# Performance work log

Measured on AMD Instinct MI355X. Metric: run time of the kernel, lower is better.

## Reference

```python
import jax, jax.numpy as jnp
import numpy as np

B, T, N = 32, 2048, 2048
D, L, TE, H = 512, 256, 1024, 8

def _ln(x, g, b, eps=1e-5):
    m = x.mean(-1, keepdims=True)
    v = ((x - m) ** 2).mean(-1, keepdims=True)
    return (x - m) / jnp.sqrt(v + eps) * g + b

def setup_inputs() -> dict:
    key = jax.random.key(0)
    ks = jax.random.split(key, 12)
    s = 0.02
    return {
        "x": jax.random.normal(ks[0], (B, T, D), jnp.float32),
        "xf": jax.random.normal(ks[1], (B, N, L), jnp.float32),
        "emb": jax.random.normal(ks[2], (B, TE), jnp.float32),
        "norm_g": jnp.ones((D,), jnp.float32),
        "norm_b": jnp.zeros((D,), jnp.float32),
        "tnorm_g": jnp.ones((L,), jnp.float32),
        "tnorm_b": jnp.zeros((L,), jnp.float32),
        "Wq": jax.random.normal(ks[3], (D, D), jnp.float32) * s,
        "bq": jnp.zeros((D,), jnp.float32),
        "Wk": jax.random.normal(ks[4], (L, D), jnp.float32) * s,
        "bk": jnp.zeros((D,), jnp.float32),
        "Wv": jax.random.normal(ks[5], (L, D), jnp.float32) * s,
        "bv": jnp.zeros((D,), jnp.float32),
        "We": jax.random.normal(ks[6], (TE, 2 * D), jnp.float32) * s,
        "be": jnp.zeros((2 * D,), jnp.float32),
        "snorm_g": jnp.ones((D,), jnp.float32),
        "snorm_b": jnp.zeros((D,), jnp.float32),
        "Wo": jax.random.normal(ks[7], (D, D), jnp.float32) * s,
        "bo": jnp.zeros((D,), jnp.float32),
    }

def reference(x, xf, emb, norm_g, norm_b, tnorm_g, tnorm_b, Wq, bq, Wk, bk, Wv, bv,
              We, be, snorm_g, snorm_b, Wo, bo):
    b, t, d = x.shape
    n = xf.shape[1]
    hd = d // H
    # projections with pre-LayerNorms
    q = (_ln(x, norm_g, norm_b) @ Wq + bq).reshape(b, t, H, hd)
    xfn = _ln(xf, tnorm_g, tnorm_b)
    k = (xfn @ Wk + bk).reshape(b, n, H, hd)
    v = (xfn @ Wv + bv).reshape(b, n, H, hd)
    # dual softmax of linear attention: query over head-dim, key over sequence
    q = jax.nn.softmax(q, axis=-1)
    k = jax.nn.softmax(k, axis=1)
    # O(N*d^2) linear attention
    attn = jnp.einsum('bnhd,bnhl->bhdl', k, v)          # [B,H,hd,hd]
    y = jnp.einsum('bthd,bhdl->bthl', q, attn).reshape(b, t, d)
    # StylizationBlock (dropout is identity in eval)
    emb_out = jax.nn.silu(emb) @ We + be                # [B, 2D]
    scale, shift = emb_out[:, None, :d], emb_out[:, None, d:]
    h = _ln(y, snorm_g, snorm_b) * (1.0 + scale) + shift
    h = jax.nn.silu(h) @ Wo + bo
    return x + h
```

## Files before the change

### kernel.cpp

```cpp
#include <hip/hip_runtime.h>
#include <math.h>

#define B_ 32
#define T_ 2048
#define N_ 2048
#define D_ 512
#define L_ 256
#define TE_ 1024
#define H_ 8
#define MROWS 65536
#define KCH 16
#define NC_ 8

typedef __attribute__((ext_vector_type(8))) short short8;
typedef __attribute__((ext_vector_type(4))) float f32x4;

__device__ __forceinline__ unsigned short f2bf(float f) {
  unsigned u = __float_as_uint(f);
  unsigned r = (u + 0x7FFF + ((u >> 16) & 1)) >> 16;
  return (unsigned short)r;
}
__device__ __forceinline__ float bf2f(unsigned short u) {
  return __uint_as_float(((unsigned)u) << 16);
}
__device__ __forceinline__ void gload_lds16(const void* g, void* l) {
  __builtin_amdgcn_global_load_lds(
      (const __attribute__((address_space(1))) void*)g,
      (__attribute__((address_space(3))) void*)l, 16, 0, 0);
}

__device__ __forceinline__ float blockReduceSum(float v, float* ws) {
#pragma unroll
  for (int m = 32; m >= 1; m >>= 1) v += __shfl_xor(v, m, 64);
  int wid = threadIdx.x >> 6;
  int lane = threadIdx.x & 63;
  __syncthreads();
  if (lane == 0) ws[wid] = v;
  __syncthreads();
  return ws[0] + ws[1] + ws[2] + ws[3];
}

template <int COLS>
__global__ void __launch_bounds__(256) ln_rows(const float* __restrict__ in,
                                               const float* __restrict__ g,
                                               const float* __restrict__ bb,
                                               unsigned short* __restrict__ out) {
  constexpr int E = COLS / 256;
  __shared__ float ws[4];
  size_t row = blockIdx.x;
  const float* rp = in + row * COLS;
  float v[E];
  float s = 0.f;
#pragma unroll
  for (int e = 0; e < E; ++e) {
    v[e] = rp[threadIdx.x + e * 256];
    s += v[e];
  }
  s = blockReduceSum(s, ws);
  float mean = s * (1.0f / COLS);
  float q = 0.f;
#pragma unroll
  for (int e = 0; e < E; ++e) {
    float d = v[e] - mean;
    q += d * d;
  }
  q = blockReduceSum(q, ws);
  float rstd = rsqrtf(q * (1.0f / COLS) + 1e-5f);
  unsigned short* op = out + row * COLS;
#pragma unroll
  for (int e = 0; e < E; ++e) {
    int c = threadIdx.x + e * 256;
    op[c] = f2bf((v[e] - mean) * rstd * g[c] + bb[c]);
  }
}

__global__ void __launch_bounds__(256) transcast(const float* __restrict__ W,
                                                 unsigned short* __restrict__ Wt,
                                                 int K, int Ncols) {
  __shared__ float t[32][33];
  int k0 = blockIdx.x * 32, n0 = blockIdx.y * 32;
  int tx = threadIdx.x & 31, ty = threadIdx.x >> 5;
#pragma unroll
  for (int i = 0; i < 32; i += 8)
    t[ty + i][tx] = W[(size_t)(k0 + ty + i) * Ncols + n0 + tx];
  __syncthreads();
#pragma unroll
  for (int i = 0; i < 32; i += 8)
    Wt[(size_t)(n0 + ty + i) * K + k0 + tx] = f2bf(t[tx][ty + i]);
}

template <int KT, bool ADD, bool OUTBF>
__global__ void __launch_bounds__(256) gemm_mfma(const unsigned short* __restrict__ A,
                                                 const unsigned short* __restrict__ Wt,
                                                 const float* __restrict__ bias,
                                                 const float* __restrict__ add,
                                                 void* __restrict__ Cv) {
  __shared__ __align__(16) unsigned short sA[128 * 32];
  __shared__ __align__(16) unsigned short sB[128 * 32];
  int tid = threadIdx.x;
  int w = tid >> 6, lane = tid & 63;
  int quad = lane >> 4, r16 = lane & 15;
  int wr = w >> 1, wc = w & 1;
  size_t m0 = (size_t)blockIdx.y * 128;
  int n0 = blockIdx.x * 128;
  int srow = lane >> 2;
  int scol = (lane & 3) * 8;
  f32x4 acc[4][4] = {};

  for (int k0 = 0; k0 < KT; k0 += 32) {
    __syncthreads();
#pragma unroll
    for (int i = 0; i < 2; ++i) {
      int seg = w * 2 + i;
      gload_lds16(&A[(m0 + seg * 16 + srow) * KT + k0 + scol], &sA[seg * 512]);
    }
#pragma unroll
    for (int i = 0; i < 2; ++i) {
      int seg = w * 2 + i;
      gload_lds16(&Wt[(size_t)(n0 + seg * 16 + srow) * KT + k0 + scol], &sB[seg * 512]);
    }
    __syncthreads();
    short8 af[4], bfr[4];
#pragma unroll
    for (int mi = 0; mi < 4; ++mi)
      af[mi] = *(const short8*)&sA[(wr * 64 + mi * 16 + r16) * 32 + quad * 8];
#pragma unroll
    for (int ni = 0; ni < 4; ++ni)
      bfr[ni] = *(const short8*)&sB[(wc * 64 + ni * 16 + r16) * 32 + quad * 8];
#pragma unroll
    for (int mi = 0; mi < 4; ++mi)
#pragma unroll
      for (int ni = 0; ni < 4; ++ni)
        acc[mi][ni] = __builtin_amdgcn_mfma_f32_16x16x32_bf16(af[mi], bfr[ni], acc[mi][ni], 0, 0, 0);
  }

  float* Cf = (float*)Cv;
  unsigned short* Cb = (unsigned short*)Cv;
#pragma unroll
  for (int mi = 0; mi < 4; ++mi)
#pragma unroll
    for (int r = 0; r < 4; ++r) {
      size_t grow = m0 + wr * 64 + mi * 16 + quad * 4 + r;
#pragma unroll
      for (int ni = 0; ni < 4; ++ni) {
        int gcol = n0 + wc * 64 + ni * 16 + r16;
        float val = acc[mi][ni][r] + bias[gcol];
        if constexpr (ADD) val += add[grow * 512 + gcol];
        if constexpr (OUTBF)
          Cb[grow * 512 + gcol] = f2bf(val);
        else
          Cf[grow * 512 + gcol] = val;
      }
    }
}

__global__ void __launch_bounds__(256) kstats_part(const float* __restrict__ k,
                                                   float* __restrict__ pmax,
                                                   float* __restrict__ psum) {
  int b = blockIdx.x, cg = blockIdx.y, ch = blockIdx.z;
  int tid = threadIdx.x;
  int lane = tid & 63, slice = tid >> 6;
  int c = cg * 64 + lane;
  constexpr int ROWS = N_ / KCH;
  constexpr int PT = ROWS / 4;
  const float* kp = k + ((size_t)b * N_ + (size_t)ch * ROWS) * D_ + c;
  float v[PT];
#pragma unroll
  for (int i = 0; i < PT; ++i) v[i] = kp[(size_t)(slice + i * 4) * D_];
  float m = v[0];
#pragma unroll
  for (int i = 1; i < PT; ++i) m = fmaxf(m, v[i]);
  float s = 0.f;
#pragma unroll
  for (int i = 0; i < PT; ++i) s += expf(v[i] - m);
  __shared__ float mred[256], sred[256];
  mred[tid] = m;
  sred[tid] = s;
  __syncthreads();
  if (tid < 64) {
    float m0 = mred[tid], m1 = mred[tid + 64], m2 = mred[tid + 128], m3 = mred[tid + 192];
    float mm = fmaxf(fmaxf(m0, m1), fmaxf(m2, m3));
    float ss = sred[tid] * expf(m0 - mm) + sred[tid + 64] * expf(m1 - mm) +
               sred[tid + 128] * expf(m2 - mm) + sred[tid + 192] * expf(m3 - mm);
    pmax[((size_t)b * KCH + ch) * D_ + cg * 64 + tid] = mm;
    psum[((size_t)b * KCH + ch) * D_ + cg * 64 + tid] = ss;
  }
}

__global__ void __launch_bounds__(256) kstats_comb(const float* __restrict__ pmax,
                                                   const float* __restrict__ psum,
                                                   float* __restrict__ kmax,
                                                   float* __restrict__ ksum) {
  int b = blockIdx.x;
  int c = blockIdx.y * 256 + threadIdx.x;
  float pm[KCH];
#pragma unroll
  for (int ch = 0; ch < KCH; ++ch) pm[ch] = pmax[((size_t)b * KCH + ch) * D_ + c];
  float m = pm[0];
#pragma unroll
  for (int ch = 1; ch < KCH; ++ch) m = fmaxf(m, pm[ch]);
  float s = 0.f;
#pragma unroll
  for (int ch = 0; ch < KCH; ++ch)
    s += psum[((size_t)b * KCH + ch) * D_ + c] * expf(pm[ch] - m);
  kmax[b * D_ + c] = m;
  ksum[b * D_ + c] = s;
}

__global__ void __launch_bounds__(256) attn_part_kernel(const float* __restrict__ k,
                                                        const float* __restrict__ v,
                                                        const float* __restrict__ kmax,
                                                        const float* __restrict__ ksum,
                                                        float* __restrict__ part) {
  int b = blockIdx.x, h = blockIdx.y, nc = blockIdx.z;
  int tid = threadIdx.x;
  __shared__ float ks_[32][68];
  __shared__ float vs_[32][68];
  __shared__ float mx[64], is_[64];
  if (tid < 64) {
    mx[tid] = kmax[b * D_ + h * 64 + tid];
    is_[tid] = 1.f / ksum[b * D_ + h * 64 + tid];
  }
  const float* kp = k + ((size_t)b * N_ + nc * 256) * D_ + h * 64;
  const float* vp = v + ((size_t)b * N_ + nc * 256) * D_ + h * 64;
  float acc[4][4] = {};
  int tx = tid & 15, ty = tid >> 4;
  int lr = tid >> 4;
  int c4 = (tid & 15) * 4;
  for (int n0 = 0; n0 < 256; n0 += 32) {
    __syncthreads();
#pragma unroll
    for (int rr = 0; rr < 32; rr += 16) {
      float4 kv = *(const float4*)&kp[(size_t)(n0 + lr + rr) * D_ + c4];
      float4 vv = *(const float4*)&vp[(size_t)(n0 + lr + rr) * D_ + c4];
      ks_[lr + rr][c4 + 0] = expf(kv.x - mx[c4 + 0]) * is_[c4 + 0];
      ks_[lr + rr][c4 + 1] = expf(kv.y - mx[c4 + 1]) * is_[c4 + 1];
      ks_[lr + rr][c4 + 2] = expf(kv.z - mx[c4 + 2]) * is_[c4 + 2];
      ks_[lr + rr][c4 + 3] = expf(kv.w - mx[c4 + 3]) * is_[c4 + 3];
      vs_[lr + rr][c4 + 0] = vv.x;
      vs_[lr + rr][c4 + 1] = vv.y;
      vs_[lr + rr][c4 + 2] = vv.z;
      vs_[lr + rr][c4 + 3] = vv.w;
    }
    __syncthreads();
#pragma unroll
    for (int nn = 0; nn < 32; ++nn) {
      float av[4], bv2[4];
#pragma unroll
      for (int i = 0; i < 4; ++i) av[i] = ks_[nn][ty * 4 + i];
#pragma unroll
      for (int j = 0; j < 4; ++j) bv2[j] = vs_[nn][tx * 4 + j];
#pragma unroll
      for (int i = 0; i < 4; ++i)
#pragma unroll
        for (int j = 0; j < 4; ++j) acc[i][j] += av[i] * bv2[j];
    }
  }
  float* ap = part + ((size_t)(b * H_ + h) * NC_ + nc) * 4096;
#pragma unroll
  for (int i = 0; i < 4; ++i) {
    float4 st = make_float4(acc[i][0], acc[i][1], acc[i][2], acc[i][3]);
    *(float4*)&ap[(ty * 4 + i) * 64 + tx * 4] = st;
  }
}

__global__ void __launch_bounds__(256) attn_reduce(const float* __restrict__ part,
                                                   float* __restrict__ attn) {
  size_t o = ((size_t)blockIdx.x * 256 + threadIdx.x) * 4;
  size_t bh = o >> 12;
  size_t e = o & 4095;
  float4 s = make_float4(0.f, 0.f, 0.f, 0.f);
#pragma unroll
  for (int nc = 0; nc < NC_; ++nc) {
    float4 p = *(const float4*)&part[(bh * NC_ + nc) * 4096 + e];
    s.x += p.x;
    s.y += p.y;
    s.z += p.z;
    s.w += p.w;
  }
  *(float4*)&attn[o] = s;
}

__global__ void __launch_bounds__(256) embmod(const float* __restrict__ emb,
                                              const float* __restrict__ We,
                                              const float* __restrict__ be,
                                              float* __restrict__ eo) {
  int b = blockIdx.x, tid = threadIdx.x;
  __shared__ float se[TE_];
  for (int i = tid; i < TE_; i += 256) {
    float e = emb[b * TE_ + i];
    se[i] = e / (1.f + expf(-e));
  }
  __syncthreads();
  int j0 = tid * 4;
  float a0 = 0, a1 = 0, a2 = 0, a3 = 0;
  for (int i = 0; i < TE_; ++i) {
    float s = se[i];
    float4 wv = *(const float4*)&We[(size_t)i * 1024 + j0];
    a0 += s * wv.x;
    a1 += s * wv.y;
    a2 += s * wv.z;
    a3 += s * wv.w;
  }
  eo[b * 1024 + j0 + 0] = a0 + be[j0 + 0];
  eo[b * 1024 + j0 + 1] = a1 + be[j0 + 1];
  eo[b * 1024 + j0 + 2] = a2 + be[j0 + 2];
  eo[b * 1024 + j0 + 3] = a3 + be[j0 + 3];
}

__global__ void __launch_bounds__(256) yein(const unsigned short* __restrict__ q,
                                            const float* __restrict__ attn,
                                            float* __restrict__ y) {
  int t0 = blockIdx.x * 32, h = blockIdx.y, b = blockIdx.z;
  int tid = threadIdx.x;
  __shared__ float at[64][68];
  __shared__ float qs[32][68];
  const float* ap = attn + (size_t)(b * H_ + h) * 4096;
  for (int i = tid; i < 4096; i += 256) at[i >> 6][i & 63] = ap[i];
  const unsigned short* qp = q + ((size_t)b * T_ + t0) * D_ + h * 64;
  for (int i = tid; i < 2048; i += 256)
    qs[i >> 6][i & 63] = bf2f(qp[(size_t)(i >> 6) * D_ + (i & 63)]);
  __syncthreads();
  int r = tid >> 3, c0 = (tid & 7) * 8;
  float lv[8];
#pragma unroll
  for (int j = 0; j < 8; ++j) lv[j] = qs[r][c0 + j];
  float m = lv[0];
#pragma unroll
  for (int j = 1; j < 8; ++j) m = fmaxf(m, lv[j]);
#pragma unroll
  for (int s = 4; s >= 1; s >>= 1) m = fmaxf(m, __shfl_xor(m, s, 64));
  float ssum = 0.f;
#pragma unroll
  for (int j = 0; j < 8; ++j) {
    lv[j] = expf(lv[j] - m);
    ssum += lv[j];
  }
#pragma unroll
  for (int s = 4; s >= 1; s >>= 1) ssum += __shfl_xor(ssum, s, 64);
  float inv = 1.f / ssum;
#pragma unroll
  for (int j = 0; j < 8; ++j) qs[r][c0 + j] = lv[j];
  __syncthreads();
  float acc[8] = {};
#pragma unroll
  for (int d = 0; d < 64; ++d) {
    float qv = qs[r][d];
#pragma unroll
    for (int j = 0; j < 8; ++j) acc[j] += qv * at[d][c0 + j];
  }
  float* yp = y + ((size_t)b * T_ + t0 + r) * D_ + h * 64 + c0;
#pragma unroll
  for (int j = 0; j < 8; ++j) yp[j] = acc[j] * inv;
}

__global__ void __launch_bounds__(256) modln(const float* __restrict__ y,
                                             const float* __restrict__ sg,
                                             const float* __restrict__ sb,
                                             const float* __restrict__ eo,
                                             unsigned short* __restrict__ hs) {
  __shared__ float ws[4];
  size_t row = blockIdx.x;
  int b = (int)(row >> 11);
  const float* rp = y + row * D_;
  float v[2];
  float s = 0.f;
#pragma unroll
  for (int e = 0; e < 2; ++e) {
    v[e] = rp[threadIdx.x + e * 256];
    s += v[e];
  }
  s = blockReduceSum(s, ws);
  float mean = s * (1.0f / D_);
  float q = 0.f;
#pragma unroll
  for (int e = 0; e < 2; ++e) {
    float d = v[e] - mean;
    q += d * d;
  }
  q = blockReduceSum(q, ws);
  float rstd = rsqrtf(q * (1.0f / D_) + 1e-5f);
#pragma unroll
  for (int e = 0; e < 2; ++e) {
    int c = threadIdx.x + e * 256;
    float xm = (v[e] - mean) * rstd * sg[c] + sb[c];
    float sc = eo[b * 1024 + c];
    float sh = eo[b * 1024 + D_ + c];
    float hm = xm * (1.f + sc) + sh;
    hs[row * D_ + c] = f2bf(hm / (1.f + expf(-hm)));
  }
}

extern "C" void kernel_launch(void* const* d_in, const int* in_sizes, int n_in,
                              void* d_out, int out_size, void* d_ws, size_t ws_size,
                              hipStream_t stream) {
  const float* x = (const float*)d_in[0];
  const float* xf = (const float*)d_in[1];
  const float* emb = (const float*)d_in[2];
  const float* norm_g = (const float*)d_in[3];
  const float* norm_b = (const float*)d_in[4];
  const float* tnorm_g = (const float*)d_in[5];
  const float* tnorm_b = (const float*)d_in[6];
  const float* Wq = (const float*)d_in[7];
  const float* bq = (const float*)d_in[8];
  const float* Wk = (const float*)d_in[9];
  const float* bk = (const float*)d_in[10];
  const float* Wv = (const float*)d_in[11];
  const float* bv = (const float*)d_in[12];
  const float* We = (const float*)d_in[13];
  const float* be = (const float*)d_in[14];
  const float* sg = (const float*)d_in[15];
  const float* sb = (const float*)d_in[16];
  const float* Wo = (const float*)d_in[17];
  const float* bo = (const float*)d_in[18];
  float* out = (float*)d_out;

  float* w = (float*)d_ws;
  unsigned short* qbf = (unsigned short*)w;
  float* kbuf = w + 16777216;
  float* vbuf = w + 16777216 + 33554432;
  unsigned short* xnbf = (unsigned short*)(w + 83886080);
  unsigned short* xfnbf = (unsigned short*)(w + 100663296);
  float* attn = w + 109051904;
  float* kmaxp = attn + 1048576;
  float* ksump = kmaxp + 16384;
  float* embout = ksump + 16384;
  unsigned short* wqt = (unsigned short*)(embout + 32768);
  unsigned short* wkt = wqt + 262144;
  unsigned short* wvt = wkt + 131072;
  unsigned short* wot = wvt + 131072;
  float* pmaxp = w + 83886080;
  float* psump = pmaxp + (size_t)B_ * KCH * D_;
  float* attnpart = w + 100663296;

  transcast<<<dim3(16, 16), 256, 0, stream>>>(Wq, wqt, 512, 512);
  transcast<<<dim3(8, 16), 256, 0, stream>>>(Wk, wkt, 256, 512);
  transcast<<<dim3(8, 16), 256, 0, stream>>>(Wv, wvt, 256, 512);
  transcast<<<dim3(16, 16), 256, 0, stream>>>(Wo, wot, 512, 512);
  ln_rows<512><<<MROWS, 256, 0, stream>>>(x, norm_g, norm_b, xnbf);
  gemm_mfma<512, false, true><<<dim3(4, 512), 256, 0, stream>>>(xnbf, wqt, bq, nullptr, qbf);
  ln_rows<256><<<MROWS, 256, 0, stream>>>(xf, tnorm_g, tnorm_b, xfnbf);
  gemm_mfma<256, false, false><<<dim3(4, 512), 256, 0, stream>>>(xfnbf, wkt, bk, nullptr, kbuf);
  gemm_mfma<256, false, false><<<dim3(4, 512), 256, 0, stream>>>(xfnbf, wvt, bv, nullptr, vbuf);
  kstats_part<<<dim3(32, 8, KCH), 256, 0, stream>>>(kbuf, pmaxp, psump);
  kstats_comb<<<dim3(32, 2), 256, 0, stream>>>(pmaxp, psump, kmaxp, ksump);
  attn_part_kernel<<<dim3(32, 8, NC_), 256, 0, stream>>>(kbuf, vbuf, kmaxp, ksump, attnpart);
  attn_reduce<<<1024, 256, 0, stream>>>(attnpart, attn);
  embmod<<<32, 256, 0, stream>>>(emb, We, be, embout);
  yein<<<dim3(64, 8, 32), 256, 0, stream>>>(qbf, attn, kbuf);
  modln<<<MROWS, 256, 0, stream>>>(kbuf, sg, sb, embout, xnbf);
  gemm_mfma<512, true, false><<<dim3(4, 512), 256, 0, stream>>>(xnbf, wot, bo, x, out);
}
```

Baseline: 946.0 us.

## Fuse query softmax into Q GEMM epilogue and run y-einsum on MFMA

The per-head query softmax now runs in the Q projection GEMM epilogue, using cross-lane shuffles over the 64 columns each wave holds for a head, and writes normalized bf16 q. attn_reduce writes the attention matrix transposed in bf16, so a new MFMA kernel (yein_mfma) can compute q·attn with bf16 matrix instructions instead of the scalar FP32 loop. This removes the softmax pass and the scalar FMA work from the yein stage. In exchange, the attention matrix and the post-softmax q are rounded to bf16, which costs some accuracy.

Result: no change. 941.1 us (-0.5%).

```diff
diff --git a/kernel.cpp b/kernel.cpp
--- a/kernel.cpp
+++ b/kernel.cpp
@@ -89,7 +89,7 @@
     Wt[(size_t)(n0 + ty + i) * K + k0 + tx] = f2bf(t[tx][ty + i]);
 }
 
-template <int KT, bool ADD, bool OUTBF>
+template <int KT, bool ADD, bool OUTBF, bool QSM>
 __global__ void __launch_bounds__(256) gemm_mfma(const unsigned short* __restrict__ A,
                                                  const unsigned short* __restrict__ Wt,
                                                  const float* __restrict__ bias,
@@ -141,15 +141,41 @@
 #pragma unroll
     for (int r = 0; r < 4; ++r) {
       size_t grow = m0 + wr * 64 + mi * 16 + quad * 4 + r;
-#pragma unroll
-      for (int ni = 0; ni < 4; ++ni) {
-        int gcol = n0 + wc * 64 + ni * 16 + r16;
-        float val = acc[mi][ni][r] + bias[gcol];
-        if constexpr (ADD) val += add[grow * 512 + gcol];
-        if constexpr (OUTBF)
-          Cb[grow * 512 + gcol] = f2bf(val);
-        else
-          Cf[grow * 512 + gcol] = val;
+      if constexpr (QSM) {
+        float v4[4];
+        float mx = -1e30f;
+#pragma unroll
+        for (int ni = 0; ni < 4; ++ni) {
+          v4[ni] = acc[mi][ni][r] + bias[n0 + wc * 64 + ni * 16 + r16];
+          mx = fmaxf(mx, v4[ni]);
+        }
+#pragma unroll
+        for (int s = 8; s >= 1; s >>= 1) mx = fmaxf(mx, __shfl_xor(mx, s, 64));
+        float ssum = 0.f;
+#pragma unroll
+        for (int ni = 0; ni < 4; ++ni) {
+          v4[ni] = expf(v4[ni] - mx);
+          ssum += v4[ni];
+        }
+#pragma unroll
+        for (int s = 8; s >= 1; s >>= 1) ssum += __shfl_xor(ssum, s, 64);
+        float inv = 1.f / ssum;
+#pragma unroll
+        for (int ni = 0; ni < 4; ++ni) {
+          int gcol = n0 + wc * 64 + ni * 16 + r16;
+          Cb[grow * 512 + gcol] = f2bf(v4[ni] * inv);
+        }
+      } else {
+#pragma unroll
+        for (int ni = 0; ni < 4; ++ni) {
+          int gcol = n0 + wc * 64 + ni * 16 + r16;
+          float val = acc[mi][ni][r] + bias[gcol];
+          if constexpr (ADD) val += add[grow * 512 + gcol];
+          if constexpr (OUTBF)
+            Cb[grow * 512 + gcol] = f2bf(val);
+          else
+            Cf[grow * 512 + gcol] = val;
+        }
       }
     }
 }
@@ -265,7 +291,7 @@
 }
 
 __global__ void __launch_bounds__(256) attn_reduce(const float* __restrict__ part,
-                                                   float* __restrict__ attn) {
+                                                   unsigned short* __restrict__ attnT) {
   size_t o = ((size_t)blockIdx.x * 256 + threadIdx.x) * 4;
   size_t bh = o >> 12;
   size_t e = o & 4095;
@@ -278,7 +304,13 @@
     s.z += p.z;
     s.w += p.w;
   }
-  *(float4*)&attn[o] = s;
+  int d = (int)(e >> 6);
+  int l = (int)(e & 63);
+  unsigned short* ab = attnT + bh * 4096;
+  ab[(l + 0) * 64 + d] = f2bf(s.x);
+  ab[(l + 1) * 64 + d] = f2bf(s.y);
+  ab[(l + 2) * 64 + d] = f2bf(s.z);
+  ab[(l + 3) * 64 + d] = f2bf(s.w);
 }
 
 __global__ void __launch_bounds__(256) embmod(const float* __restrict__ emb,
@@ -308,50 +340,54 @@
   eo[b * 1024 + j0 + 3] = a3 + be[j0 + 3];
 }
 
-__global__ void __launch_bounds__(256) yein(const unsigned short* __restrict__ q,
-                                            const float* __restrict__ attn,
-                                            float* __restrict__ y) {
-  int t0 = blockIdx.x * 32, h = blockIdx.y, b = blockIdx.z;
+__global__ void __launch_bounds__(256) yein_mfma(const unsigned short* __restrict__ qsm,
+                                                 const unsigned short* __restrict__ attnT,
+                                                 float* __restrict__ y) {
+  int b = blockIdx.z, h = blockIdx.y;
+  size_t t0 = (size_t)blockIdx.x * 256;
   int tid = threadIdx.x;
-  __shared__ float at[64][68];
-  __shared__ float qs[32][68];
-  const float* ap = attn + (size_t)(b * H_ + h) * 4096;
-  for (int i = tid; i < 4096; i += 256) at[i >> 6][i & 63] = ap[i];
-  const unsigned short* qp = q + ((size_t)b * T_ + t0) * D_ + h * 64;
-  for (int i = tid; i < 2048; i += 256)
-    qs[i >> 6][i & 63] = bf2f(qp[(size_t)(i >> 6) * D_ + (i & 63)]);
-  __syncthreads();
-  int r = tid >> 3, c0 = (tid & 7) * 8;
-  float lv[8];
-#pragma unroll
-  for (int j = 0; j < 8; ++j) lv[j] = qs[r][c0 + j];
-  float m = lv[0];
-#pragma unroll
-  for (int j = 1; j < 8; ++j) m = fmaxf(m, lv[j]);
-#pragma unroll
-  for (int s = 4; s >= 1; s >>= 1) m = fmaxf(m, __shfl_xor(m, s, 64));
-  float ssum = 0.f;
-#pragma unroll
-  for (int j = 0; j < 8; ++j) {
-    lv[j] = expf(lv[j] - m);
-    ssum += lv[j];
-  }
-#pragma unroll
-  for (int s = 4; s >= 1; s >>= 1) ssum += __shfl_xor(ssum, s, 64);
-  float inv = 1.f / ssum;
-#pragma unroll
-  for (int j = 0; j < 8; ++j) qs[r][c0 + j] = lv[j];
-  __syncthreads();
-  float acc[8] = {};
-#pragma unroll
-  for (int d = 0; d < 64; ++d) {
-    float qv = qs[r][d];
-#pragma unroll
-    for (int j = 0; j < 8; ++j) acc[j] += qv * at[d][c0 + j];
-  }
-  float* yp = y + ((size_t)b * T_ + t0 + r) * D_ + h * 64 + c0;
-#pragma unroll
-  for (int j = 0; j < 8; ++j) yp[j] = acc[j] * inv;
+  int w = tid >> 6, lane = tid & 63;
+  int quad = lane >> 4, r16 = lane & 15;
+  int srow = lane >> 2;
+  int scol = (lane & 3) * 8;
+  __shared__ __align__(16) unsigned short sA[256 * 32];
+  __shared__ __align__(16) unsigned short sB[64 * 32];
+  const unsigned short* qp = qsm + ((size_t)b * T_ + t0) * D_ + h * 64;
+  const unsigned short* bp = attnT + (size_t)(b * H_ + h) * 4096;
+  f32x4 acc[4][4] = {};
+
+  for (int k0 = 0; k0 < 64; k0 += 32) {
+    __syncthreads();
+#pragma unroll
+    for (int i = 0; i < 4; ++i) {
+      int seg = w * 4 + i;
+      gload_lds16(&qp[(size_t)(seg * 16 + srow) * D_ + k0 + scol], &sA[seg * 512]);
+    }
+    gload_lds16(&bp[(w * 16 + srow) * 64 + k0 + scol], &sB[w * 512]);
+    __syncthreads();
+    short8 af[4], bfr[4];
+#pragma unroll
+    for (int mi = 0; mi < 4; ++mi)
+      af[mi] = *(const short8*)&sA[(w * 64 + mi * 16 + r16) * 32 + quad * 8];
+#pragma unroll
+    for (int ni = 0; ni < 4; ++ni)
+      bfr[ni] = *(const short8*)&sB[(ni * 16 + r16) * 32 + quad * 8];
+#pragma unroll
+    for (int mi = 0; mi < 4; ++mi)
+#pragma unroll
+      for (int ni = 0; ni < 4; ++ni)
+        acc[mi][ni] = __builtin_amdgcn_mfma_f32_16x16x32_bf16(af[mi], bfr[ni], acc[mi][ni], 0, 0, 0);
+  }
+
+#pragma unroll
+  for (int mi = 0; mi < 4; ++mi)
+#pragma unroll
+    for (int r = 0; r < 4; ++r) {
+      size_t grow = t0 + w * 64 + mi * 16 + quad * 4 + r;
+      float* yp = y + ((size_t)b * T_ + grow) * D_ + h * 64;
+#pragma unroll
+      for (int ni = 0; ni < 4; ++ni) yp[ni * 16 + r16] = acc[mi][ni][r];
+    }
 }
 
 __global__ void __launch_bounds__(256) modln(const float* __restrict__ y,
@@ -421,8 +457,8 @@
   float* vbuf = w + 16777216 + 33554432;
   unsigned short* xnbf = (unsigned short*)(w + 83886080);
   unsigned short* xfnbf = (unsigned short*)(w + 100663296);
-  float* attn = w + 109051904;
-  float* kmaxp = attn + 1048576;
+  unsigned short* attnT = (unsigned short*)(w + 109051904);
+  float* kmaxp = w + 109051904 + 1048576;
   float* ksump = kmaxp + 16384;
   float* embout = ksump + 16384;
   unsigned short* wqt = (unsigned short*)(embout + 32768);
@@ -438,16 +474,16 @@
   transcast<<<dim3(8, 16), 256, 0, stream>>>(Wv, wvt, 256, 512);
   transcast<<<dim3(16, 16), 256, 0, stream>>>(Wo, wot, 512, 512);
   ln_rows<512><<<MROWS, 256, 0, stream>>>(x, norm_g, norm_b, xnbf);
-  gemm_mfma<512, false, true><<<dim3(4, 512), 256, 0, stream>>>(xnbf, wqt, bq, nullptr, qbf);
+  gemm_mfma<512, false, true, true><<<dim3(4, 512), 256, 0, stream>>>(xnbf, wqt, bq, nullptr, qbf);
   ln_rows<256><<<MROWS, 256, 0, stream>>>(xf, tnorm_g, tnorm_b, xfnbf);
-  gemm_mfma<256, false, false><<<dim3(4, 512), 256, 0, stream>>>(xfnbf, wkt, bk, nullptr, kbuf);
-  gemm_mfma<256, false, false><<<dim3(4, 512), 256, 0, stream>>>(xfnbf, wvt, bv, nullptr, vbuf);
+  gemm_mfma<256, false, false, false><<<dim3(4, 512), 256, 0, stream>>>(xfnbf, wkt, bk, nullptr, kbuf);
+  gemm_mfma<256, false, false, false><<<dim3(4, 512), 256, 0, stream>>>(xfnbf, wvt, bv, nullptr, vbuf);
   kstats_part<<<dim3(32, 8, KCH), 256, 0, stream>>>(kbuf, pmaxp, psump);
   kstats_comb<<<dim3(32, 2), 256, 0, stream>>>(pmaxp, psump, kmaxp, ksump);
   attn_part_kernel<<<dim3(32, 8, NC_), 256, 0, stream>>>(kbuf, vbuf, kmaxp, ksump, attnpart);
-  attn_reduce<<<1024, 256, 0, stream>>>(attnpart, attn);
+  attn_reduce<<<1024, 256, 0, stream>>>(attnpart, attnT);
   embmod<<<32, 256, 0, stream>>>(emb, We, be, embout);
-  yein<<<dim3(64, 8, 32), 256, 0, stream>>>(qbf, attn, kbuf);
+  yein_mfma<<<dim3(8, 8, 32), 256, 0, stream>>>(qbf, attnT, kbuf);
   modln<<<MROWS, 256, 0, stream>>>(kbuf, sg, sb, embout, xnbf);
-  gemm_mfma<512, true, false><<<dim3(4, 512), 256, 0, stream>>>(xnbf, wot, bo, x, out);
-}
+  gemm_mfma<512, true, false, false><<<dim3(4, 512), 256, 0, stream>>>(xnbf, wot, bo, x, out);
+}
```
